# Performance work log

Measured on AMD Instinct MI355X. Metric: run time of the kernel, lower is better.

The kernel has to match this reference:

```python
import jax, jax.numpy as jnp
import numpy as np
import math

B, S, D, H = 2, 2048, 2048, 16
DH = D // H  # head dim = 128
THETA = 10000.0


def _rope(x, pos):
    """Interleaved RoPE. x: [..., S, DH], pos: [S] (int)."""
    dh = x.shape[-1]
    freqs = (1.0 / THETA) ** (2.0 * jnp.arange(dh // 2, dtype=jnp.float32) / dh)  # [DH/2]
    ang = pos.astype(jnp.float32)[:, None] * freqs[None, :]  # [S, DH/2]
    cos = jnp.cos(ang).astype(x.dtype)
    sin = jnp.sin(ang).astype(x.dtype)
    xe = x[..., 0::2]
    xo = x[..., 1::2]
    oe = xe * cos - xo * sin
    oo = xe * sin + xo * cos
    return jnp.stack([oe, oo], axis=-1).reshape(x.shape)


def setup_inputs() -> dict:
    key = jax.random.key(0)
    ks = jax.random.split(key, 5)
    std = 2.0 / math.sqrt(D + D)
    x = jax.random.normal(ks[0], (B, S, D), dtype=jnp.float32)
    Wq = jax.random.normal(ks[1], (D, D), dtype=jnp.float32) * std
    Wk = jax.random.normal(ks[2], (D, D), dtype=jnp.float32) * std
    Wv = jax.random.normal(ks[3], (D, D), dtype=jnp.float32) * std
    Wo = jax.random.normal(ks[4], (D, D), dtype=jnp.float32) * std
    token_positions = jnp.arange(S, dtype=jnp.int64 if jax.config.jax_enable_x64 else jnp.int32)[None, :]
    return {"x": x, "token_positions": token_positions, "Wq": Wq, "Wk": Wk, "Wv": Wv, "Wo": Wo}


def reference(x, token_positions, Wq, Wk, Wv, Wo):
    b, s, d = x.shape
    pos = token_positions[0]  # [S]
    # QKV projections (Linear is x @ W.T, no bias)
    Q = (x @ Wq.T).reshape(b, s, H, DH).transpose(0, 2, 1, 3)  # [b,h,s,dh]
    K = (x @ Wk.T).reshape(b, s, H, DH).transpose(0, 2, 1, 3)
    V = (x @ Wv.T).reshape(b, s, H, DH).transpose(0, 2, 1, 3)
    # per-head RoPE on Q and K
    Q = _rope(Q, pos)
    K = _rope(K, pos)
    # scaled dot-product attention with causal mask
    scores = jnp.einsum('bhqd,bhkd->bhqk', Q, K) / math.sqrt(DH)
    causal = jnp.tril(jnp.ones((s, s), dtype=bool))  # [s,s]
    scores = jnp.where(causal[None, None, :, :], scores, -jnp.inf)
    prob = jax.nn.softmax(scores, axis=-1)
    O = jnp.einsum('bhqk,bhkd->bhqd', prob, V)  # [b,h,s,dh]
    O = O.transpose(0, 2, 1, 3).reshape(b, s, d)
    return O @ Wo.T
```

## Files before the change

### kernel.cpp

```cpp
#include <hip/hip_runtime.h>
#include <hip/hip_bf16.h>
#include <math.h>

#define BB 2
#define SS 2048
#define DD 2048
#define HH 16
#define DHH 128
#define MM (BB*SS)

typedef __attribute__((ext_vector_type(8))) short bf16x8;
typedef __attribute__((ext_vector_type(4))) float f32x4;

#define AS1 __attribute__((address_space(1)))
#define AS3 __attribute__((address_space(3)))
#define GLOAD_LDS16(g, l) __builtin_amdgcn_global_load_lds((const AS1 void*)(g), (AS3 void*)(l), 16, 0, 0)

__device__ __forceinline__ float b2f(short s) {
  union { unsigned int u; float f; } v;
  v.u = ((unsigned int)(unsigned short)s) << 16;
  return v.f;
}
__device__ __forceinline__ short f2b(float f) {
  union { float f; unsigned int u; } v; v.f = f;
  unsigned int u = v.u;
  u += 0x7fffu + ((u >> 16) & 1u);
  return (short)(u >> 16);
}
__device__ __forceinline__ short f2b_fast(float f) {
  union { float f; unsigned int u; } v; v.f = f;
  return (short)((v.u + 0x8000u) >> 16);
}

template<int CTRL>
__device__ __forceinline__ float dppf(float x) {
  int xi = __builtin_bit_cast(int, x);
  int r = __builtin_amdgcn_update_dpp(0, xi, CTRL, 0xf, 0xf, true);
  return __builtin_bit_cast(float, r);
}
__device__ __forceinline__ float rmax16(float x) {
  x = fmaxf(x, dppf<0xB1>(x));
  x = fmaxf(x, dppf<0x4E>(x));
  x = fmaxf(x, dppf<0x141>(x));
  x = fmaxf(x, dppf<0x140>(x));
  return x;
}
__device__ __forceinline__ float rsum16(float x) {
  x += dppf<0xB1>(x);
  x += dppf<0x4E>(x);
  x += dppf<0x141>(x);
  x += dppf<0x140>(x);
  return x;
}

__global__ void cvt_all(const float* __restrict__ x,  const float* __restrict__ wq,
                        const float* __restrict__ wk, const float* __restrict__ wv,
                        const float* __restrict__ wo,
                        short* __restrict__ xb,  short* __restrict__ wqb,
                        short* __restrict__ wkb, short* __restrict__ wvb,
                        short* __restrict__ wob) {
  int i = blockIdx.x * blockDim.x + threadIdx.x;
  const float* src; short* dst; int off;
  if (i < 2097152) { src = x; dst = xb; off = i; }
  else {
    int j = i - 2097152;
    int w = j >> 20; off = j & 1048575;
    src = (w == 0) ? wq : (w == 1) ? wk : (w == 2) ? wv : wo;
    dst = (w == 0) ? wqb : (w == 1) ? wkb : (w == 2) ? wvb : wob;
  }
  float4 v = ((const float4*)src)[i < 2097152 ? off : off];
  short4 o;
  o.x = f2b(v.x); o.y = f2b(v.y); o.z = f2b(v.z); o.w = f2b(v.w);
  ((short4*)dst)[off] = o;
}

__global__ __launch_bounds__(256, 2)
void gemm_qkv(const short* __restrict__ A,
              const short* __restrict__ Wq, const short* __restrict__ Wk,
              const short* __restrict__ Wv, const int* __restrict__ pos,
              short* __restrict__ Qo, short* __restrict__ Ko, short* __restrict__ Vo) {
  __shared__ __align__(16) short As[256*64];
  __shared__ __align__(16) short Bs[128*64];
  const int tid = threadIdx.x;
  const int lane = tid & 63;
  const int wave = tid >> 6;
  const int quad = lane >> 4, l16 = lane & 15;
  const int wsel = blockIdx.x >> 4;
  const short* Bw = Wq; short* Cout = Qo;
  if (wsel == 1) { Bw = Wk; Cout = Ko; }
  else if (wsel == 2) { Bw = Wv; Cout = Vo; }
  const int bn = (blockIdx.x & 15) * 128;
  const int bm = blockIdx.y * 256;
  const int K = DD;

  const int srow = tid >> 3;
  const int scol = (tid & 7) * 8;
  const short* aBase = A + (size_t)(bm + srow) * K + scol;
  const short* bBase = Bw + (size_t)(bn + srow) * K + scol;
  f32x4 acc[4][8] = {};

  for (int k0 = 0; k0 < K; k0 += 64) {
    #pragma unroll
    for (int j = 0; j < 8; ++j)
      GLOAD_LDS16(aBase + (size_t)j * 32 * K + k0, As + j * 2048 + wave * 512);
    #pragma unroll
    for (int j = 0; j < 4; ++j)
      GLOAD_LDS16(bBase + (size_t)j * 32 * K + k0, Bs + j * 2048 + wave * 512);
    __syncthreads();
    #pragma unroll
    for (int kk = 0; kk < 64; kk += 32) {
      bf16x8 af[4], bf[8];
      #pragma unroll
      for (int t = 0; t < 4; ++t)
        af[t] = *(const bf16x8*)&As[(wave*64 + t*16 + l16) * 64 + kk + quad*8];
      #pragma unroll
      for (int t = 0; t < 8; ++t)
        bf[t] = *(const bf16x8*)&Bs[(t*16 + l16) * 64 + kk + quad*8];
      #pragma unroll
      for (int mt = 0; mt < 4; ++mt)
        #pragma unroll
        for (int nt = 0; nt < 8; ++nt)
          acc[mt][nt] = __builtin_amdgcn_mfma_f32_16x16x32_bf16(af[mt], bf[nt], acc[mt][nt], 0, 0, 0);
    }
    __syncthreads();
  }

  if (wsel < 2) {
    const float post = (wsel == 0) ? 0.08838834764831845f : 1.0f;
    float fr[8];
    #pragma unroll
    for (int nt = 0; nt < 8; ++nt) {
      int pi = nt*8 + (l16 >> 1);
      fr[nt] = __expf(-0.14391156831f * (float)pi);
    }
    const float sgn = (l16 & 1) ? 1.0f : -1.0f;
    #pragma unroll
    for (int mt = 0; mt < 4; ++mt) {
      #pragma unroll
      for (int r = 0; r < 4; ++r) {
        int m = bm + wave*64 + mt*16 + quad*4 + r;
        float fp = (float)pos[m & 2047];
        #pragma unroll
        for (int nt = 0; nt < 8; ++nt) {
          float v = acc[mt][nt][r];
          float p = dppf<0xB1>(v);
          float ang = fp * fr[nt];
          float sn = __sinf(ang), cs = __cosf(ang);
          acc[mt][nt][r] = (v * cs + sgn * p * sn) * post;
        }
      }
    }
  }

  #pragma unroll
  for (int mt = 0; mt < 4; ++mt)
    #pragma unroll
    for (int nt = 0; nt < 8; ++nt)
      #pragma unroll
      for (int r = 0; r < 4; ++r) {
        int m = bm + wave*64 + mt*16 + quad*4 + r;
        int n = bn + nt*16 + l16;
        int b = m >> 11, s = m & 2047;
        int h = n >> 7,  d = n & 127;
        Cout[(((size_t)(b*HH + h)*SS + s)*DHH) + d] = f2b(acc[mt][nt][r]);
      }
}

__global__ __launch_bounds__(256)
void gemm_o(const short* __restrict__ A, const short* __restrict__ Bw,
            float* __restrict__ Cout) {
  __shared__ __align__(16) short As[128*64];
  __shared__ __align__(16) short Bs[128*64];
  const int tid = threadIdx.x;
  const int lane = tid & 63;
  const int wave = tid >> 6;
  const int wm = wave >> 1, wn = wave & 1;
  const int quad = lane >> 4, l16 = lane & 15;
  const int bm = blockIdx.y * 128, bn = blockIdx.x * 128;
  const int K = DD;

  const int srow = tid >> 3;
  const int scol = (tid & 7) * 8;
  const short* aBase = A + (size_t)(bm + srow) * K + scol;
  const short* bBase = Bw + (size_t)(bn + srow) * K + scol;
  f32x4 acc[4][4] = {};

  for (int k0 = 0; k0 < K; k0 += 64) {
    #pragma unroll
    for (int j = 0; j < 4; ++j) {
      GLOAD_LDS16(aBase + (size_t)j * 32 * K + k0, As + j * 2048 + wave * 512);
      GLOAD_LDS16(bBase + (size_t)j * 32 * K + k0, Bs + j * 2048 + wave * 512);
    }
    __syncthreads();
    #pragma unroll
    for (int kk = 0; kk < 64; kk += 32) {
      bf16x8 af[4], bf[4];
      #pragma unroll
      for (int t = 0; t < 4; ++t)
        af[t] = *(const bf16x8*)&As[(wm*64 + t*16 + l16) * 64 + kk + quad*8];
      #pragma unroll
      for (int t = 0; t < 4; ++t)
        bf[t] = *(const bf16x8*)&Bs[(wn*64 + t*16 + l16) * 64 + kk + quad*8];
      #pragma unroll
      for (int mt = 0; mt < 4; ++mt)
        #pragma unroll
        for (int nt = 0; nt < 4; ++nt)
          acc[mt][nt] = __builtin_amdgcn_mfma_f32_16x16x32_bf16(af[mt], bf[nt], acc[mt][nt], 0, 0, 0);
    }
    __syncthreads();
  }

  #pragma unroll
  for (int mt = 0; mt < 4; ++mt)
    #pragma unroll
    for (int nt = 0; nt < 4; ++nt)
      #pragma unroll
      for (int r = 0; r < 4; ++r) {
        int m = bm + wm*64 + mt*16 + quad*4 + r;
        int n = bn + wn*64 + nt*16 + l16;
        Cout[(size_t)m * DD + n] = acc[mt][nt][r];
      }
}

__global__ __launch_bounds__(256, 2)
void attn(const short* __restrict__ Q, const short* __restrict__ K,
          const short* __restrict__ V, short* __restrict__ O) {
  __shared__ __align__(16) short Ks[64*136];
  __shared__ __align__(16) short Vt[128*72];
  __shared__ __align__(16) short Pb[4*32*72];
  const int tid = threadIdx.x;
  const int lane = tid & 63, wave = tid >> 6;
  const int quad = lane >> 4, l16 = lane & 15;
  const int p = blockIdx.x;
  const int qa = p, qb = 31 - p;
  const int bh = blockIdx.y;
  const int b = bh >> 4, h = bh & 15;
  const short* Kg = K + (size_t)bh * SS * DHH;
  const short* Vg = V + (size_t)bh * SS * DHH;

  bf16x8 aq[2][4];
  #pragma unroll
  for (int t = 0; t < 2; ++t) {
    int qrb = (t ? qb : qa) * 64;
    const short* qp = Q + ((size_t)bh * SS + qrb + wave*16 + l16) * DHH + quad*8;
    #pragma unroll
    for (int ks = 0; ks < 4; ++ks) aq[t][ks] = *(const bf16x8*)(qp + ks*32);
  }

  f32x4 o[2][8] = {};
  float mrow[2][4], lrow[2][4];
  #pragma unroll
  for (int t = 0; t < 2; ++t)
    #pragma unroll
    for (int r = 0; r < 4; ++r) { mrow[t][r] = -1e30f; lrow[t][r] = 0.f; }

  const int krow = tid >> 2;
  const int kseg = (tid & 3) * 32;
  const int vkp  = (tid & 31) * 2;
  const int vds  = (tid >> 5) * 16;

  const int nkt = qb + 1;
  int4 kreg[4], vreg[4];
  {
    const short* kp = Kg + (size_t)krow * DHH + kseg;
    #pragma unroll
    for (int j = 0; j < 4; ++j) kreg[j] = *(const int4*)(kp + j*8);
    const short* vp = Vg + (size_t)vkp * DHH + vds;
    vreg[0] = *(const int4*)(vp);
    vreg[1] = *(const int4*)(vp + 8);
    vreg[2] = *(const int4*)(vp + DHH);
    vreg[3] = *(const int4*)(vp + DHH + 8);
  }

  for (int kt = 0; kt < nkt; ++kt) {
    #pragma unroll
    for (int j = 0; j < 4; ++j)
      *(int4*)&Ks[krow*136 + kseg + j*8] = kreg[j];
    {
      const short* s0 = (const short*)&vreg[0];
      const short* s1 = (const short*)&vreg[2];
      #pragma unroll
      for (int e = 0; e < 16; ++e) {
        int val = (int)(unsigned short)s0[e] | ((int)(unsigned short)s1[e] << 16);
        *(int*)&Vt[(vds + e)*72 + vkp] = val;
      }
    }
    __syncthreads();

    if (kt + 1 < nkt) {
      const short* kp = Kg + (size_t)((kt+1)*64 + krow) * DHH + kseg;
      #pragma unroll
      for (int j = 0; j < 4; ++j) kreg[j] = *(const int4*)(kp + j*8);
      const short* vp = Vg + (size_t)((kt+1)*64 + vkp) * DHH + vds;
      vreg[0] = *(const int4*)(vp);
      vreg[1] = *(const int4*)(vp + 8);
      vreg[2] = *(const int4*)(vp + DHH);
      vreg[3] = *(const int4*)(vp + DHH + 8);
    }

    const bool actA = (kt <= qa);

    float sv[2][4][4];
    #pragma unroll
    for (int nt = 0; nt < 4; ++nt) {
      f32x4 a1 = {0.f,0.f,0.f,0.f}, a0 = {0.f,0.f,0.f,0.f};
      #pragma unroll
      for (int ks = 0; ks < 4; ++ks) {
        bf16x8 bk = *(const bf16x8*)&Ks[(nt*16 + l16)*136 + ks*32 + quad*8];
        a1 = __builtin_amdgcn_mfma_f32_16x16x32_bf16(aq[1][ks], bk, a1, 0, 0, 0);
        if (actA) a0 = __builtin_amdgcn_mfma_f32_16x16x32_bf16(aq[0][ks], bk, a0, 0, 0, 0);
      }
      #pragma unroll
      for (int r = 0; r < 4; ++r) {
        sv[1][nt][r] = a1[r];
        sv[0][nt][r] = a0[r];
      }
    }
    #pragma unroll
    for (int t = 0; t < 2; ++t) {
      int tq = t ? qb : qa;
      if (kt == tq) {
        #pragma unroll
        for (int nt = 0; nt < 4; ++nt)
          #pragma unroll
          for (int r = 0; r < 4; ++r)
            if (nt*16 + l16 > wave*16 + quad*4 + r) sv[t][nt][r] = -1e30f;
      }
    }

    #pragma unroll
    for (int t = 0; t < 2; ++t) {
      if (t == 0 && !actA) continue;
      #pragma unroll
      for (int r = 0; r < 4; ++r) {
        float mx = fmaxf(fmaxf(sv[t][0][r], sv[t][1][r]), fmaxf(sv[t][2][r], sv[t][3][r]));
        mx = rmax16(mx);
        float mnew = fmaxf(mrow[t][r], mx);
        float alpha = __expf(mrow[t][r] - mnew);
        float ls = 0.f;
        #pragma unroll
        for (int nt = 0; nt < 4; ++nt) {
          float pv = __expf(sv[t][nt][r] - mnew);
          sv[t][nt][r] = pv; ls += pv;
        }
        ls = rsum16(ls);
        lrow[t][r] = lrow[t][r] * alpha + ls;
        mrow[t][r] = mnew;
        #pragma unroll
        for (int nt = 0; nt < 8; ++nt) o[t][nt][r] *= alpha;
      }
      #pragma unroll
      for (int nt = 0; nt < 4; ++nt)
        #pragma unroll
        for (int r = 0; r < 4; ++r)
          Pb[wave*2304 + (t*16 + quad*4 + r)*72 + nt*16 + l16] = f2b_fast(sv[t][nt][r]);
    }

    bf16x8 ap[2][2];
    #pragma unroll
    for (int t = 0; t < 2; ++t)
      #pragma unroll
      for (int k2 = 0; k2 < 2; ++k2)
        ap[t][k2] = *(const bf16x8*)&Pb[wave*2304 + (t*16 + l16)*72 + k2*32 + quad*8];
    #pragma unroll
    for (int k2 = 0; k2 < 2; ++k2) {
      #pragma unroll
      for (int nt = 0; nt < 8; ++nt) {
        bf16x8 bv = *(const bf16x8*)&Vt[(nt*16 + l16)*72 + k2*32 + quad*8];
        o[1][nt] = __builtin_amdgcn_mfma_f32_16x16x32_bf16(ap[1][k2], bv, o[1][nt], 0, 0, 0);
        if (actA) o[0][nt] = __builtin_amdgcn_mfma_f32_16x16x32_bf16(ap[0][k2], bv, o[0][nt], 0, 0, 0);
      }
    }
    __syncthreads();
  }

  #pragma unroll
  for (int t = 0; t < 2; ++t) {
    int qrb = (t ? qb : qa) * 64;
    #pragma unroll
    for (int nt = 0; nt < 8; ++nt)
      #pragma unroll
      for (int r = 0; r < 4; ++r) {
        int q = qrb + wave*16 + quad*4 + r;
        float v = o[t][nt][r] / lrow[t][r];
        O[((size_t)(b*SS + q)) * DD + h*DHH + nt*16 + l16] = f2b(v);
      }
  }
}

extern "C" void kernel_launch(void* const* d_in, const int* in_sizes, int n_in,
                              void* d_out, int out_size, void* d_ws, size_t ws_size,
                              hipStream_t stream) {
  const float* x  = (const float*)d_in[0];
  const int* pos  = (const int*)d_in[1];
  const float* Wq = (const float*)d_in[2];
  const float* Wk = (const float*)d_in[3];
  const float* Wv = (const float*)d_in[4];
  const float* Wo = (const float*)d_in[5];

  char* ws = (char*)d_ws;
  short* xb  = (short*)(ws);
  short* wqb = (short*)(ws + 16777216);
  short* wkb = (short*)(ws + 25165824);
  short* wvb = (short*)(ws + 33554432);
  short* wob = (short*)(ws + 41943040);
  short* Qb  = (short*)(ws + 50331648);
  short* Kb  = (short*)(ws + 67108864);
  short* Vb  = (short*)(ws + 83886080);
  short* Ob  = (short*)(ws + 100663296);

  cvt_all<<<24576, 256, 0, stream>>>(x, Wq, Wk, Wv, Wo, xb, wqb, wkb, wvb, wob);

  dim3 gq(48, MM/256);
  gemm_qkv<<<gq, 256, 0, stream>>>(xb, wqb, wkb, wvb, pos, Qb, Kb, Vb);

  dim3 ga(16, BB*HH);
  attn<<<ga, 256, 0, stream>>>(Qb, Kb, Vb, Ob);

  dim3 go(DD/128, MM/128);
  gemm_o<<<go, 256, 0, stream>>>(Ob, wob, (float*)d_out);
}
```

Baseline: 464.8 us.

## Split attention q-tile pair across 8 waves with XOR-swizzled LDS and exp2 softmax

The attention block grows from 4 to 8 waves: each wave now owns one 16-row slice of a single q-tile instead of two, which halves per-wave accumulator registers and targets higher occupancy. The padded LDS layouts are replaced with XOR-swizzled unpadded ones to avoid bank conflicts. The Q scale folds in log2(e) so softmax can use native exp2, and setprio is placed around the MFMA sections. Waves assigned to the short q-tile sit idle for the later key tiles, and each wave still waits at every block barrier.

Result: faster. 443.6 us (-4.6%).

```diff
diff --git a/kernel.cpp b/kernel.cpp
--- a/kernel.cpp
+++ b/kernel.cpp
@@ -15,6 +15,12 @@
 #define AS1 __attribute__((address_space(1)))
 #define AS3 __attribute__((address_space(3)))
 #define GLOAD_LDS16(g, l) __builtin_amdgcn_global_load_lds((const AS1 void*)(g), (AS3 void*)(l), 16, 0, 0)
+
+#if __has_builtin(__builtin_amdgcn_exp2f)
+#define EXP2F(x) __builtin_amdgcn_exp2f(x)
+#else
+#define EXP2F(x) exp2f(x)
+#endif
 
 __device__ __forceinline__ float b2f(short s) {
   union { unsigned int u; float f; } v;
@@ -126,7 +132,7 @@
   }
 
   if (wsel < 2) {
-    const float post = (wsel == 0) ? 0.08838834764831845f : 1.0f;
+    const float post = (wsel == 0) ? 0.1275174306f : 1.0f;
     float fr[8];
     #pragma unroll
     for (int nt = 0; nt < 8; ++nt) {
@@ -222,12 +228,12 @@
       }
 }
 
-__global__ __launch_bounds__(256, 2)
+__global__ __launch_bounds__(512, 4)
 void attn(const short* __restrict__ Q, const short* __restrict__ K,
           const short* __restrict__ V, short* __restrict__ O) {
-  __shared__ __align__(16) short Ks[64*136];
-  __shared__ __align__(16) short Vt[128*72];
-  __shared__ __align__(16) short Pb[4*32*72];
+  __shared__ __align__(16) short Ks[64*128];
+  __shared__ __align__(16) short Vt[128*64];
+  __shared__ __align__(16) short Pb[8*16*64];
   const int tid = threadIdx.x;
   const int lane = tid & 63, wave = tid >> 6;
   const int quad = lane >> 4, l16 = lane & 15;
@@ -238,154 +244,142 @@
   const short* Kg = K + (size_t)bh * SS * DHH;
   const short* Vg = V + (size_t)bh * SS * DHH;
 
-  bf16x8 aq[2][4];
+  const int wt = wave >> 2;
+  const int qtile = wt ? qb : qa;
+  const int qbase = qtile * 64 + (wave & 3) * 16;
+
+  bf16x8 aq[4];
+  {
+    const short* qp = Q + ((size_t)bh * SS + qbase + l16) * DHH + quad*8;
+    #pragma unroll
+    for (int ks = 0; ks < 4; ++ks) aq[ks] = *(const bf16x8*)(qp + ks*32);
+  }
+
+  f32x4 o[8] = {};
+  float mrow[4], lrow[4];
   #pragma unroll
-  for (int t = 0; t < 2; ++t) {
-    int qrb = (t ? qb : qa) * 64;
-    const short* qp = Q + ((size_t)bh * SS + qrb + wave*16 + l16) * DHH + quad*8;
-    #pragma unroll
-    for (int ks = 0; ks < 4; ++ks) aq[t][ks] = *(const bf16x8*)(qp + ks*32);
-  }
-
-  f32x4 o[2][8] = {};
-  float mrow[2][4], lrow[2][4];
-  #pragma unroll
-  for (int t = 0; t < 2; ++t)
-    #pragma unroll
-    for (int r = 0; r < 4; ++r) { mrow[t][r] = -1e30f; lrow[t][r] = 0.f; }
-
-  const int krow = tid >> 2;
-  const int kseg = (tid & 3) * 32;
-  const int vkp  = (tid & 31) * 2;
-  const int vds  = (tid >> 5) * 16;
+  for (int r = 0; r < 4; ++r) { mrow[r] = -1e30f; lrow[r] = 0.f; }
+
+  const int krow = tid >> 3;
+  const int kcolb = (tid & 7) * 32;
+  const int vkp = (tid & 31) * 2;
+  const int vds = (tid >> 5) * 8;
 
   const int nkt = qb + 1;
-  int4 kreg[4], vreg[4];
+  int4 kreg[2], vreg[2];
   {
-    const short* kp = Kg + (size_t)krow * DHH + kseg;
-    #pragma unroll
-    for (int j = 0; j < 4; ++j) kreg[j] = *(const int4*)(kp + j*8);
+    const short* kp = Kg + (size_t)krow * DHH + (kcolb >> 1);
+    kreg[0] = *(const int4*)kp; kreg[1] = *(const int4*)(kp + 8);
     const short* vp = Vg + (size_t)vkp * DHH + vds;
-    vreg[0] = *(const int4*)(vp);
-    vreg[1] = *(const int4*)(vp + 8);
-    vreg[2] = *(const int4*)(vp + DHH);
-    vreg[3] = *(const int4*)(vp + DHH + 8);
+    vreg[0] = *(const int4*)vp; vreg[1] = *(const int4*)(vp + DHH);
   }
 
   for (int kt = 0; kt < nkt; ++kt) {
     #pragma unroll
-    for (int j = 0; j < 4; ++j)
-      *(int4*)&Ks[krow*136 + kseg + j*8] = kreg[j];
+    for (int j = 0; j < 2; ++j)
+      *(int4*)((char*)Ks + krow*256 + ((kcolb + j*16) ^ ((krow & 7) << 4))) = kreg[j];
     {
       const short* s0 = (const short*)&vreg[0];
-      const short* s1 = (const short*)&vreg[2];
-      #pragma unroll
-      for (int e = 0; e < 16; ++e) {
+      const short* s1 = (const short*)&vreg[1];
+      #pragma unroll
+      for (int e = 0; e < 8; ++e) {
+        int dim = vds + e;
         int val = (int)(unsigned short)s0[e] | ((int)(unsigned short)s1[e] << 16);
-        *(int*)&Vt[(vds + e)*72 + vkp] = val;
+        *(int*)((char*)Vt + dim*128 + ((vkp*2) ^ ((dim & 7) << 4))) = val;
       }
     }
     __syncthreads();
 
     if (kt + 1 < nkt) {
-      const short* kp = Kg + (size_t)((kt+1)*64 + krow) * DHH + kseg;
-      #pragma unroll
-      for (int j = 0; j < 4; ++j) kreg[j] = *(const int4*)(kp + j*8);
+      const short* kp = Kg + (size_t)((kt+1)*64 + krow) * DHH + (kcolb >> 1);
+      kreg[0] = *(const int4*)kp; kreg[1] = *(const int4*)(kp + 8);
       const short* vp = Vg + (size_t)((kt+1)*64 + vkp) * DHH + vds;
-      vreg[0] = *(const int4*)(vp);
-      vreg[1] = *(const int4*)(vp + 8);
-      vreg[2] = *(const int4*)(vp + DHH);
-      vreg[3] = *(const int4*)(vp + DHH + 8);
-    }
-
-    const bool actA = (kt <= qa);
-
-    float sv[2][4][4];
-    #pragma unroll
-    for (int nt = 0; nt < 4; ++nt) {
-      f32x4 a1 = {0.f,0.f,0.f,0.f}, a0 = {0.f,0.f,0.f,0.f};
-      #pragma unroll
-      for (int ks = 0; ks < 4; ++ks) {
-        bf16x8 bk = *(const bf16x8*)&Ks[(nt*16 + l16)*136 + ks*32 + quad*8];
-        a1 = __builtin_amdgcn_mfma_f32_16x16x32_bf16(aq[1][ks], bk, a1, 0, 0, 0);
-        if (actA) a0 = __builtin_amdgcn_mfma_f32_16x16x32_bf16(aq[0][ks], bk, a0, 0, 0, 0);
-      }
-      #pragma unroll
-      for (int r = 0; r < 4; ++r) {
-        sv[1][nt][r] = a1[r];
-        sv[0][nt][r] = a0[r];
-      }
-    }
-    #pragma unroll
-    for (int t = 0; t < 2; ++t) {
-      int tq = t ? qb : qa;
-      if (kt == tq) {
+      vreg[0] = *(const int4*)vp; vreg[1] = *(const int4*)(vp + DHH);
+    }
+
+    if (kt <= qtile) {
+      float sv[4][4];
+      __builtin_amdgcn_s_setprio(1);
+      #pragma unroll
+      for (int nt = 0; nt < 4; ++nt) {
+        f32x4 a = {0.f, 0.f, 0.f, 0.f};
+        #pragma unroll
+        for (int ks = 0; ks < 4; ++ks) {
+          int key = nt*16 + l16;
+          bf16x8 bk = *(const bf16x8*)((const char*)Ks + key*256 +
+                         ((ks*64 + quad*16) ^ ((key & 7) << 4)));
+          a = __builtin_amdgcn_mfma_f32_16x16x32_bf16(aq[ks], bk, a, 0, 0, 0);
+        }
+        #pragma unroll
+        for (int r = 0; r < 4; ++r) sv[nt][r] = a[r];
+      }
+      __builtin_amdgcn_s_setprio(0);
+
+      if (kt == qtile) {
         #pragma unroll
         for (int nt = 0; nt < 4; ++nt)
           #pragma unroll
           for (int r = 0; r < 4; ++r)
-            if (nt*16 + l16 > wave*16 + quad*4 + r) sv[t][nt][r] = -1e30f;
-      }
-    }
-
-    #pragma unroll
-    for (int t = 0; t < 2; ++t) {
-      if (t == 0 && !actA) continue;
+            if (nt*16 + l16 > (wave & 3)*16 + quad*4 + r) sv[nt][r] = -1e30f;
+      }
+
       #pragma unroll
       for (int r = 0; r < 4; ++r) {
-        float mx = fmaxf(fmaxf(sv[t][0][r], sv[t][1][r]), fmaxf(sv[t][2][r], sv[t][3][r]));
+        float mx = fmaxf(fmaxf(sv[0][r], sv[1][r]), fmaxf(sv[2][r], sv[3][r]));
         mx = rmax16(mx);
-        float mnew = fmaxf(mrow[t][r], mx);
-        float alpha = __expf(mrow[t][r] - mnew);
+        float mnew = fmaxf(mrow[r], mx);
+        float alpha = EXP2F(mrow[r] - mnew);
         float ls = 0.f;
         #pragma unroll
         for (int nt = 0; nt < 4; ++nt) {
-          float pv = __expf(sv[t][nt][r] - mnew);
-          sv[t][nt][r] = pv; ls += pv;
+          float pv = EXP2F(sv[nt][r] - mnew);
+          sv[nt][r] = pv; ls += pv;
         }
         ls = rsum16(ls);
-        lrow[t][r] = lrow[t][r] * alpha + ls;
-        mrow[t][r] = mnew;
-        #pragma unroll
-        for (int nt = 0; nt < 8; ++nt) o[t][nt][r] *= alpha;
-      }
+        lrow[r] = lrow[r] * alpha + ls;
+        mrow[r] = mnew;
+        #pragma unroll
+        for (int nt = 0; nt < 8; ++nt) o[nt][r] *= alpha;
+      }
+
       #pragma unroll
       for (int nt = 0; nt < 4; ++nt)
         #pragma unroll
-        for (int r = 0; r < 4; ++r)
-          Pb[wave*2304 + (t*16 + quad*4 + r)*72 + nt*16 + l16] = f2b_fast(sv[t][nt][r]);
-    }
-
-    bf16x8 ap[2][2];
-    #pragma unroll
-    for (int t = 0; t < 2; ++t)
+        for (int r = 0; r < 4; ++r) {
+          int qr = quad*4 + r;
+          *(short*)((char*)Pb + wave*2048 + qr*128 +
+                    (((nt*16 + l16)*2) ^ ((qr & 7) << 4))) = f2b_fast(sv[nt][r]);
+        }
+
+      bf16x8 ap[2];
       #pragma unroll
       for (int k2 = 0; k2 < 2; ++k2)
-        ap[t][k2] = *(const bf16x8*)&Pb[wave*2304 + (t*16 + l16)*72 + k2*32 + quad*8];
-    #pragma unroll
-    for (int k2 = 0; k2 < 2; ++k2) {
-      #pragma unroll
-      for (int nt = 0; nt < 8; ++nt) {
-        bf16x8 bv = *(const bf16x8*)&Vt[(nt*16 + l16)*72 + k2*32 + quad*8];
-        o[1][nt] = __builtin_amdgcn_mfma_f32_16x16x32_bf16(ap[1][k2], bv, o[1][nt], 0, 0, 0);
-        if (actA) o[0][nt] = __builtin_amdgcn_mfma_f32_16x16x32_bf16(ap[0][k2], bv, o[0][nt], 0, 0, 0);
-      }
+        ap[k2] = *(const bf16x8*)((const char*)Pb + wave*2048 + l16*128 +
+                    ((k2*64 + quad*16) ^ ((l16 & 7) << 4)));
+
+      __builtin_amdgcn_s_setprio(1);
+      #pragma unroll
+      for (int k2 = 0; k2 < 2; ++k2)
+        #pragma unroll
+        for (int nt = 0; nt < 8; ++nt) {
+          int d = nt*16 + l16;
+          bf16x8 bv = *(const bf16x8*)((const char*)Vt + d*128 +
+                         ((k2*64 + quad*16) ^ ((d & 7) << 4)));
+          o[nt] = __builtin_amdgcn_mfma_f32_16x16x32_bf16(ap[k2], bv, o[nt], 0, 0, 0);
+        }
+      __builtin_amdgcn_s_setprio(0);
     }
     __syncthreads();
   }
 
   #pragma unroll
-  for (int t = 0; t < 2; ++t) {
-    int qrb = (t ? qb : qa) * 64;
-    #pragma unroll
-    for (int nt = 0; nt < 8; ++nt)
-      #pragma unroll
-      for (int r = 0; r < 4; ++r) {
-        int q = qrb + wave*16 + quad*4 + r;
-        float v = o[t][nt][r] / lrow[t][r];
-        O[((size_t)(b*SS + q)) * DD + h*DHH + nt*16 + l16] = f2b(v);
-      }
-  }
+  for (int nt = 0; nt < 8; ++nt)
+    #pragma unroll
+    for (int r = 0; r < 4; ++r) {
+      int q = qbase + quad*4 + r;
+      float v = o[nt][r] / lrow[r];
+      O[((size_t)(b*SS + q)) * DD + h*DHH + nt*16 + l16] = f2b(v);
+    }
 }
 
 extern "C" void kernel_launch(void* const* d_in, const int* in_sizes, int n_in,
@@ -415,7 +409,7 @@
   gemm_qkv<<<gq, 256, 0, stream>>>(xb, wqb, wkb, wvb, pos, Qb, Kb, Vb);
 
   dim3 ga(16, BB*HH);
-  attn<<<ga, 256, 0, stream>>>(Qb, Kb, Vb, Ob);
+  attn<<<ga, 512, 0, stream>>>(Qb, Kb, Vb, Ob);
 
   dim3 go(DD/128, MM/128);
   gemm_o<<<go, 256, 0, stream>>>(Ob, wob, (float*)d_out);
```
